# Performance work log

Measured on AMD Instinct MI355X. Metric: run time of the kernel, lower is better.

The kernel has to match this reference:

```python
import jax, jax.numpy as jnp
import numpy as np

B, H, W, C_IN, C_QK = 8, 64, 64, 256, 32


def setup_inputs() -> dict:
    key = jax.random.key(0)
    ks = jax.random.split(key, 5)
    x = jax.random.normal(ks[0], (B, H, W, C_IN), dtype=jnp.float32)
    Wq = jax.random.normal(ks[1], (C_IN, C_QK), dtype=jnp.float32) * 0.05
    bq = jnp.zeros((C_QK,), dtype=jnp.float32)
    Wk = jax.random.normal(ks[2], (C_IN, C_QK), dtype=jnp.float32) * 0.05
    bk = jnp.zeros((C_QK,), dtype=jnp.float32)
    Wv = jax.random.normal(ks[3], (C_IN, C_IN), dtype=jnp.float32) * 0.05
    bv = jnp.zeros((C_IN,), dtype=jnp.float32)
    gamma = jax.random.normal(ks[4], (1,), dtype=jnp.float32)
    return {"x": x, "Wq": Wq, "bq": bq, "Wk": Wk, "bk": bk, "Wv": Wv, "bv": bv, "gamma": gamma}


def reference(x, Wq, bq, Wk, bk, Wv, bv, gamma):
    b, h, w, c_in = x.shape
    n = h * w
    xt = x.reshape(b, n, c_in)                      # tokens: (B, N, C_in)
    # 1x1 convs == per-token channel matmuls
    q = xt @ Wq + bq                                # (B, N, Cqk)
    k = xt @ Wk + bk                                # (B, N, Cqk)
    v = xt @ Wv + bv                                # (B, N, C_in)
    energy = jnp.einsum('bnc,bmc->bnm', q, k)       # (B, N, N)
    attn = jax.nn.softmax(energy, axis=-1)
    # original: out = (V^T @ A^T)^T == A @ V
    out = jnp.einsum('bnm,bmc->bnc', attn, v)       # (B, N, C_in)
    out = out.reshape(b, h, w, c_in)
    out = gamma * out + x                           # residual with learned scale
    return jnp.mean(out, axis=-1)                   # channel-mean pool -> (B, H, W)
```

## Files before the change

### kernel.cpp

```cpp
#include <hip/hip_runtime.h>
#include <hip/hip_bf16.h>


typedef _Float16 half8  __attribute__((ext_vector_type(8)));
typedef _Float16 half4v __attribute__((ext_vector_type(4)));
typedef float    f32x4  __attribute__((ext_vector_type(4)));

#define LOG2E 1.4426950408889634f

#if __has_builtin(__builtin_amdgcn_exp2f)
#define EXP2(x) __builtin_amdgcn_exp2f(x)
#else
#define EXP2(x) exp2f(x)
#endif

__global__ __launch_bounds__(256) void prep_kernel(
    const float* __restrict__ Wq, const float* __restrict__ Wk,
    const float* __restrict__ Wv, const float* __restrict__ bv,
    _Float16* __restrict__ Wfr, float* __restrict__ wvbar, float* __restrict__ bvbar)
{
  int bid = blockIdx.x, tid = threadIdx.x;
  if (bid < 64) {
    int col = bid, c = tid;
    float v = (col < 32) ? Wq[c * 32 + col] : Wk[c * 32 + (col - 32)];
    int ch = c >> 5, quad = (c >> 3) & 3, j = c & 7;
    Wfr[(size_t)((ch * 4 + quad) * 64 + col) * 8 + j] = (_Float16)v;
  } else if (bid < 128) {
    int row = (bid - 64) * 4 + (tid >> 6);
    int lane = tid & 63;
    const float* p = Wv + (size_t)row * 256 + lane * 4;
    float s = p[0] + p[1] + p[2] + p[3];
    #pragma unroll
    for (int off = 32; off >= 1; off >>= 1) s += __shfl_xor(s, off);
    if (lane == 0) wvbar[row] = s * (1.0f / 256.0f);
  } else {
    if (tid < 64) {
      const float* p = bv + tid * 4;
      float s = p[0] + p[1] + p[2] + p[3];
      #pragma unroll
      for (int off = 32; off >= 1; off >>= 1) s += __shfl_xor(s, off);
      if (tid == 0) bvbar[0] = s * (1.0f / 256.0f);
    }
  }
}

__global__ __launch_bounds__(256) void proj_kernel(
    const float* __restrict__ x, const _Float16* __restrict__ Wfr,
    const float* __restrict__ bq, const float* __restrict__ bk,
    const float* __restrict__ wvbar, const float* __restrict__ bvbar,
    _Float16* __restrict__ Qh, _Float16* __restrict__ Kh,
    float* __restrict__ vbarO, float* __restrict__ xbarO)
{
  __shared__ _Float16 XT[64 * 264];
  int tid = threadIdx.x, blk = blockIdx.x;
  size_t tok0 = (size_t)blk * 64;

  const float4* xg4 = (const float4*)x;
  #pragma unroll
  for (int i = 0; i < 16; ++i) {
    int f = i * 256 + tid;
    int tok = f >> 6, c4 = f & 63;
    float4 v = xg4[(size_t)blk * 4096 + f];
    half4v h;
    h.x = (_Float16)v.x; h.y = (_Float16)v.y; h.z = (_Float16)v.z; h.w = (_Float16)v.w;
    *(half4v*)&XT[tok * 264 + c4 * 4] = h;
  }
  __syncthreads();

  if (tid < 64) {
    float vs = 0.f, xs = 0.f;
    #pragma unroll 4
    for (int g = 0; g < 32; ++g) {
      half8 h = *(const half8*)&XT[tid * 264 + g * 8];
      #pragma unroll
      for (int j = 0; j < 8; ++j) {
        float xv = (float)h[j];
        vs += xv * wvbar[g * 8 + j];
        xs += xv;
      }
    }
    vbarO[tok0 + tid] = vs + bvbar[0];
    xbarO[tok0 + tid] = xs * (1.0f / 256.0f);
  }

  int lane = tid & 63, w = tid >> 6;
  int l15 = lane & 15, quad = lane >> 4;
  f32x4 acc[4] = {(f32x4){0,0,0,0},(f32x4){0,0,0,0},(f32x4){0,0,0,0},(f32x4){0,0,0,0}};
  #pragma unroll
  for (int ch = 0; ch < 8; ++ch) {
    half8 a = *(const half8*)&XT[(w * 16 + l15) * 264 + ch * 32 + quad * 8];
    #pragma unroll
    for (int ct = 0; ct < 4; ++ct) {
      half8 bf = *(const half8*)(Wfr + (size_t)((ch * 4 + quad) * 64 + ct * 16 + l15) * 8);
      acc[ct] = __builtin_amdgcn_mfma_f32_16x16x32_f16(a, bf, acc[ct], 0, 0, 0);
    }
  }
  #pragma unroll
  for (int ct = 0; ct < 4; ++ct) {
    int col = ct * 16 + l15;
    #pragma unroll
    for (int r = 0; r < 4; ++r) {
      int token = w * 16 + quad * 4 + r;
      if (ct < 2) {
        float val = (acc[ct][r] + bq[col]) * LOG2E;
        Qh[(tok0 + token) * 32 + col] = (_Float16)val;
      } else {
        float val = acc[ct][r] + bk[col - 32];
        Kh[(tok0 + token) * 32 + (col - 32)] = (_Float16)val;
      }
    }
  }
}

__global__ __launch_bounds__(256) void flash_kernel(
    const _Float16* __restrict__ Qh, const _Float16* __restrict__ Kh,
    const float* __restrict__ vbar, const float* __restrict__ xbar,
    const float* __restrict__ gamma, float* __restrict__ out)
{
  int tid = threadIdx.x, blk = blockIdx.x;
  int b = blk >> 6, qt = blk & 63;
  int lane = tid & 63, w = tid >> 6;
  int l15 = lane & 15, quad = lane >> 4;

  const _Float16* Qb = Qh + (size_t)b * 4096 * 32;
  const _Float16* Kb = Kh + (size_t)b * 4096 * 32;
  const float* vb = vbar + (size_t)b * 4096;

  int qrow = qt * 64 + w * 16 + l15;
  half8 aq = *(const half8*)(Qb + (size_t)qrow * 32 + quad * 8);

  float lacc[4] = {0, 0, 0, 0}, oacc[4] = {0, 0, 0, 0};
  const f32x4 cinit = {-88.f, -88.f, -88.f, -88.f};

  const _Float16* kfrag = Kb + (size_t)l15 * 32 + quad * 8;
  const float* vfrag = vb + l15;

  #pragma unroll 2
  for (int kt = 0; kt < 64; ++kt) {
    half8 bk8[4];
    float vbl[4];
    #pragma unroll
    for (int ct = 0; ct < 4; ++ct) {
      bk8[ct] = *(const half8*)(kfrag + (size_t)(kt * 64 + ct * 16) * 32);
      vbl[ct] = vfrag[kt * 64 + ct * 16];
    }
    f32x4 sc[4];
    #pragma unroll
    for (int ct = 0; ct < 4; ++ct)
      sc[ct] = __builtin_amdgcn_mfma_f32_16x16x32_f16(aq, bk8[ct], cinit, 0, 0, 0);
    #pragma unroll
    for (int r = 0; r < 4; ++r) {
      float p0 = EXP2(sc[0][r]), p1 = EXP2(sc[1][r]);
      float p2 = EXP2(sc[2][r]), p3 = EXP2(sc[3][r]);
      lacc[r] += (p0 + p1) + (p2 + p3);
      oacc[r] += ((p0 * vbl[0] + p1 * vbl[1]) + (p2 * vbl[2] + p3 * vbl[3]));
    }
  }

  #pragma unroll
  for (int r = 0; r < 4; ++r) {
    #pragma unroll
    for (int off = 1; off < 16; off <<= 1) {
      lacc[r] += __shfl_xor(lacc[r], off);
      oacc[r] += __shfl_xor(oacc[r], off);
    }
  }
  if (l15 == 0) {
    float g = gamma[0];
    #pragma unroll
    for (int r = 0; r < 4; ++r) {
      int row = qt * 64 + w * 16 + quad * 4 + r;
      out[(size_t)b * 4096 + row] = g * (oacc[r] / lacc[r]) + xbar[(size_t)b * 4096 + row];
    }
  }
}

extern "C" void kernel_launch(void* const* d_in, const int* in_sizes, int n_in,
                              void* d_out, int out_size, void* d_ws, size_t ws_size,
                              hipStream_t stream)
{
  const float* x     = (const float*)d_in[0];
  const float* Wq    = (const float*)d_in[1];
  const float* bq    = (const float*)d_in[2];
  const float* Wk    = (const float*)d_in[3];
  const float* bk    = (const float*)d_in[4];
  const float* Wv    = (const float*)d_in[5];
  const float* bv    = (const float*)d_in[6];
  const float* gamma = (const float*)d_in[7];
  float* out = (float*)d_out;

  char* ws = (char*)d_ws;
  _Float16* Wfr  = (_Float16*)(ws);
  float* wvbar   = (float*)(ws + 32768);
  float* bvbar   = (float*)(ws + 33792);
  _Float16* Qh   = (_Float16*)(ws + 65536);
  _Float16* Kh   = (_Float16*)(ws + 65536 + 2097152);
  float* vbarA   = (float*)(ws + 65536 + 4194304);
  float* xbarA   = (float*)(ws + 65536 + 4194304 + 131072);

  prep_kernel<<<129, 256, 0, stream>>>(Wq, Wk, Wv, bv, Wfr, wvbar, bvbar);
  proj_kernel<<<512, 256, 0, stream>>>(x, Wfr, bq, bk, wvbar, bvbar, Qh, Kh, vbarA, xbarA);
  flash_kernel<<<512, 256, 0, stream>>>(Qh, Kh, vbarA, xbarA, gamma, out);
}
```

Measured before the change: 125.8 us.

## Split flash attention over two key halves and combine partials in a new kernel

Measured after the change: 129.0 us. +2.5%, slower.

```diff
diff --git a/kernel.cpp b/kernel.cpp
--- a/kernel.cpp
+++ b/kernel.cpp
@@ -5,6 +5,7 @@
 typedef _Float16 half8  __attribute__((ext_vector_type(8)));
 typedef _Float16 half4v __attribute__((ext_vector_type(4)));
 typedef float    f32x4  __attribute__((ext_vector_type(4)));
+typedef float    f32x2  __attribute__((ext_vector_type(2)));
 
 #define LOG2E 1.4426950408889634f
 
@@ -112,13 +113,15 @@
   }
 }
 
-__global__ __launch_bounds__(256) void flash_kernel(
+__global__ __launch_bounds__(256, 4) void flash_kernel(
     const _Float16* __restrict__ Qh, const _Float16* __restrict__ Kh,
-    const float* __restrict__ vbar, const float* __restrict__ xbar,
-    const float* __restrict__ gamma, float* __restrict__ out)
+    const float* __restrict__ vbar,
+    float* __restrict__ lpart, float* __restrict__ opart)
 {
   int tid = threadIdx.x, blk = blockIdx.x;
-  int b = blk >> 6, qt = blk & 63;
+  int b = blk >> 7;
+  int qt = (blk >> 1) & 63;
+  int ks = blk & 1;
   int lane = tid & 63, w = tid >> 6;
   int l15 = lane & 15, quad = lane >> 4;
 
@@ -129,14 +132,16 @@
   int qrow = qt * 64 + w * 16 + l15;
   half8 aq = *(const half8*)(Qb + (size_t)qrow * 32 + quad * 8);
 
-  float lacc[4] = {0, 0, 0, 0}, oacc[4] = {0, 0, 0, 0};
+  f32x2 l2[4], o2[4];
+  #pragma unroll
+  for (int r = 0; r < 4; ++r) { l2[r] = (f32x2){0, 0}; o2[r] = (f32x2){0, 0}; }
   const f32x4 cinit = {-88.f, -88.f, -88.f, -88.f};
 
-  const _Float16* kfrag = Kb + (size_t)l15 * 32 + quad * 8;
-  const float* vfrag = vb + l15;
+  const _Float16* kfrag = Kb + ((size_t)ks * 2048 + l15) * 32 + quad * 8;
+  const float* vfrag = vb + ks * 2048 + l15;
 
   #pragma unroll 2
-  for (int kt = 0; kt < 64; ++kt) {
+  for (int kt = 0; kt < 32; ++kt) {
     half8 bk8[4];
     float vbl[4];
     #pragma unroll
@@ -148,14 +153,21 @@
     #pragma unroll
     for (int ct = 0; ct < 4; ++ct)
       sc[ct] = __builtin_amdgcn_mfma_f32_16x16x32_f16(aq, bk8[ct], cinit, 0, 0, 0);
+    f32x2 vA = {vbl[0], vbl[1]}, vB = {vbl[2], vbl[3]};
     #pragma unroll
     for (int r = 0; r < 4; ++r) {
       float p0 = EXP2(sc[0][r]), p1 = EXP2(sc[1][r]);
       float p2 = EXP2(sc[2][r]), p3 = EXP2(sc[3][r]);
-      lacc[r] += (p0 + p1) + (p2 + p3);
-      oacc[r] += ((p0 * vbl[0] + p1 * vbl[1]) + (p2 * vbl[2] + p3 * vbl[3]));
-    }
-  }
+      f32x2 pA = {p0, p1}, pB = {p2, p3};
+      l2[r] += pA + pB;
+      o2[r] += pA * vA;
+      o2[r] += pB * vB;
+    }
+  }
+
+  float lacc[4], oacc[4];
+  #pragma unroll
+  for (int r = 0; r < 4; ++r) { lacc[r] = l2[r].x + l2[r].y; oacc[r] = o2[r].x + o2[r].y; }
 
   #pragma unroll
   for (int r = 0; r < 4; ++r) {
@@ -166,13 +178,25 @@
     }
   }
   if (l15 == 0) {
-    float g = gamma[0];
     #pragma unroll
     for (int r = 0; r < 4; ++r) {
       int row = qt * 64 + w * 16 + quad * 4 + r;
-      out[(size_t)b * 4096 + row] = g * (oacc[r] / lacc[r]) + xbar[(size_t)b * 4096 + row];
-    }
-  }
+      size_t g = (size_t)b * 4096 + row;
+      lpart[(size_t)ks * 32768 + g] = lacc[r];
+      opart[(size_t)ks * 32768 + g] = oacc[r];
+    }
+  }
+}
+
+__global__ __launch_bounds__(256) void combine_kernel(
+    const float* __restrict__ lpart, const float* __restrict__ opart,
+    const float* __restrict__ xbar, const float* __restrict__ gamma,
+    float* __restrict__ out)
+{
+  int i = blockIdx.x * 256 + threadIdx.x;
+  float l = lpart[i] + lpart[32768 + i];
+  float o = opart[i] + opart[32768 + i];
+  out[i] = gamma[0] * (o / l) + xbar[i];
 }
 
 extern "C" void kernel_launch(void* const* d_in, const int* in_sizes, int n_in,
@@ -197,8 +221,11 @@
   _Float16* Kh   = (_Float16*)(ws + 65536 + 2097152);
   float* vbarA   = (float*)(ws + 65536 + 4194304);
   float* xbarA   = (float*)(ws + 65536 + 4194304 + 131072);
+  float* lpart   = (float*)(ws + 65536 + 4194304 + 262144);
+  float* opart   = (float*)(ws + 65536 + 4194304 + 524288);
 
   prep_kernel<<<129, 256, 0, stream>>>(Wq, Wk, Wv, bv, Wfr, wvbar, bvbar);
   proj_kernel<<<512, 256, 0, stream>>>(x, Wfr, bq, bk, wvbar, bvbar, Qh, Kh, vbarA, xbarA);
-  flash_kernel<<<512, 256, 0, stream>>>(Qh, Kh, vbarA, xbarA, gamma, out);
-}
+  flash_kernel<<<1024, 256, 0, stream>>>(Qh, Kh, vbarA, lpart, opart);
+  combine_kernel<<<128, 256, 0, stream>>>(lpart, opart, xbarA, gamma, out);
+}
```

## Fuse prep, projection and attention kernels into one persistent kernel with grid barriers

Applied to the files above, without the earlier changes.

Result: slower. 229.0 us (+82.0%).

```diff
diff --git a/kernel.cpp b/kernel.cpp
--- a/kernel.cpp
+++ b/kernel.cpp
@@ -1,5 +1,4 @@
 #include <hip/hip_runtime.h>
-#include <hip/hip_bf16.h>
 
 
 typedef _Float16 half8  __attribute__((ext_vector_type(8)));
@@ -14,26 +13,53 @@
 #define EXP2(x) exp2f(x)
 #endif
 
-__global__ __launch_bounds__(256) void prep_kernel(
-    const float* __restrict__ Wq, const float* __restrict__ Wk,
+#define NBLOCKS 512
+
+__device__ __forceinline__ void grid_barrier(int* cnt) {
+  __syncthreads();
+  if (threadIdx.x == 0) {
+    __threadfence();
+    __hip_atomic_fetch_add(cnt, 1, __ATOMIC_ACQ_REL, __HIP_MEMORY_SCOPE_AGENT);
+    long t = 0;
+    while (__hip_atomic_load(cnt, __ATOMIC_ACQUIRE, __HIP_MEMORY_SCOPE_AGENT) < NBLOCKS) {
+      if (++t > (1L << 26)) break;
+      __builtin_amdgcn_s_sleep(1);
+    }
+    __threadfence();
+  }
+  __syncthreads();
+}
+
+__global__ __launch_bounds__(256, 2) void fused_kernel(
+    const float* __restrict__ x,
+    const float* __restrict__ Wq, const float* __restrict__ bq,
+    const float* __restrict__ Wk, const float* __restrict__ bk,
     const float* __restrict__ Wv, const float* __restrict__ bv,
-    _Float16* __restrict__ Wfr, float* __restrict__ wvbar, float* __restrict__ bvbar)
+    const float* __restrict__ gamma,
+    _Float16* __restrict__ Wfr, float* __restrict__ wvbar, float* __restrict__ bvbar,
+    _Float16* __restrict__ Qh, _Float16* __restrict__ Kh,
+    float* __restrict__ vbarA, float* __restrict__ xbarA,
+    int* __restrict__ gbar,
+    float* __restrict__ out)
 {
-  int bid = blockIdx.x, tid = threadIdx.x;
-  if (bid < 64) {
-    int col = bid, c = tid;
+  __shared__ _Float16 XT[64 * 264];
+  int tid = threadIdx.x, blk = blockIdx.x;
+  int lane = tid & 63, w = tid >> 6;
+  int l15 = lane & 15, quad = lane >> 4;
+
+  if (blk < 64) {
+    int col = blk, c = tid;
     float v = (col < 32) ? Wq[c * 32 + col] : Wk[c * 32 + (col - 32)];
-    int ch = c >> 5, quad = (c >> 3) & 3, j = c & 7;
-    Wfr[(size_t)((ch * 4 + quad) * 64 + col) * 8 + j] = (_Float16)v;
-  } else if (bid < 128) {
-    int row = (bid - 64) * 4 + (tid >> 6);
-    int lane = tid & 63;
+    int ch = c >> 5, qd = (c >> 3) & 3, j = c & 7;
+    Wfr[(size_t)((ch * 4 + qd) * 64 + col) * 8 + j] = (_Float16)v;
+  } else if (blk < 128) {
+    int row = (blk - 64) * 4 + w;
     const float* p = Wv + (size_t)row * 256 + lane * 4;
     float s = p[0] + p[1] + p[2] + p[3];
     #pragma unroll
     for (int off = 32; off >= 1; off >>= 1) s += __shfl_xor(s, off);
     if (lane == 0) wvbar[row] = s * (1.0f / 256.0f);
-  } else {
+  } else if (blk == 128) {
     if (tid < 64) {
       const float* p = bv + tid * 4;
       float s = p[0] + p[1] + p[2] + p[3];
@@ -42,135 +68,122 @@
       if (tid == 0) bvbar[0] = s * (1.0f / 256.0f);
     }
   }
-}
-
-__global__ __launch_bounds__(256) void proj_kernel(
-    const float* __restrict__ x, const _Float16* __restrict__ Wfr,
-    const float* __restrict__ bq, const float* __restrict__ bk,
-    const float* __restrict__ wvbar, const float* __restrict__ bvbar,
-    _Float16* __restrict__ Qh, _Float16* __restrict__ Kh,
-    float* __restrict__ vbarO, float* __restrict__ xbarO)
-{
-  __shared__ _Float16 XT[64 * 264];
-  int tid = threadIdx.x, blk = blockIdx.x;
-  size_t tok0 = (size_t)blk * 64;
-
-  const float4* xg4 = (const float4*)x;
-  #pragma unroll
-  for (int i = 0; i < 16; ++i) {
-    int f = i * 256 + tid;
-    int tok = f >> 6, c4 = f & 63;
-    float4 v = xg4[(size_t)blk * 4096 + f];
-    half4v h;
-    h.x = (_Float16)v.x; h.y = (_Float16)v.y; h.z = (_Float16)v.z; h.w = (_Float16)v.w;
-    *(half4v*)&XT[tok * 264 + c4 * 4] = h;
-  }
-  __syncthreads();
-
-  if (tid < 64) {
-    float vs = 0.f, xs = 0.f;
-    #pragma unroll 4
-    for (int g = 0; g < 32; ++g) {
-      half8 h = *(const half8*)&XT[tid * 264 + g * 8];
-      #pragma unroll
-      for (int j = 0; j < 8; ++j) {
-        float xv = (float)h[j];
-        vs += xv * wvbar[g * 8 + j];
-        xs += xv;
-      }
-    }
-    vbarO[tok0 + tid] = vs + bvbar[0];
-    xbarO[tok0 + tid] = xs * (1.0f / 256.0f);
-  }
-
-  int lane = tid & 63, w = tid >> 6;
-  int l15 = lane & 15, quad = lane >> 4;
-  f32x4 acc[4] = {(f32x4){0,0,0,0},(f32x4){0,0,0,0},(f32x4){0,0,0,0},(f32x4){0,0,0,0}};
-  #pragma unroll
-  for (int ch = 0; ch < 8; ++ch) {
-    half8 a = *(const half8*)&XT[(w * 16 + l15) * 264 + ch * 32 + quad * 8];
+
+  grid_barrier(gbar + 0);
+
+  {
+    size_t tok0 = (size_t)blk * 64;
+
+    const float4* xg4 = (const float4*)x;
+    #pragma unroll
+    for (int i = 0; i < 16; ++i) {
+      int f = i * 256 + tid;
+      int tok = f >> 6, c4 = f & 63;
+      float4 v = xg4[(size_t)blk * 4096 + f];
+      half4v h;
+      h.x = (_Float16)v.x; h.y = (_Float16)v.y; h.z = (_Float16)v.z; h.w = (_Float16)v.w;
+      *(half4v*)&XT[tok * 264 + c4 * 4] = h;
+    }
+    __syncthreads();
+
+    if (tid < 64) {
+      float vs = 0.f, xs = 0.f;
+      #pragma unroll 4
+      for (int g = 0; g < 32; ++g) {
+        half8 h = *(const half8*)&XT[tid * 264 + g * 8];
+        #pragma unroll
+        for (int j = 0; j < 8; ++j) {
+          float xv = (float)h[j];
+          vs += xv * wvbar[g * 8 + j];
+          xs += xv;
+        }
+      }
+      vbarA[tok0 + tid] = vs + bvbar[0];
+      xbarA[tok0 + tid] = xs * (1.0f / 256.0f);
+    }
+
+    f32x4 acc[4] = {(f32x4){0,0,0,0},(f32x4){0,0,0,0},(f32x4){0,0,0,0},(f32x4){0,0,0,0}};
+    #pragma unroll
+    for (int ch = 0; ch < 8; ++ch) {
+      half8 a = *(const half8*)&XT[(w * 16 + l15) * 264 + ch * 32 + quad * 8];
+      #pragma unroll
+      for (int ct = 0; ct < 4; ++ct) {
+        half8 bf = *(const half8*)(Wfr + (size_t)((ch * 4 + quad) * 64 + ct * 16 + l15) * 8);
+        acc[ct] = __builtin_amdgcn_mfma_f32_16x16x32_f16(a, bf, acc[ct], 0, 0, 0);
+      }
+    }
     #pragma unroll
     for (int ct = 0; ct < 4; ++ct) {
-      half8 bf = *(const half8*)(Wfr + (size_t)((ch * 4 + quad) * 64 + ct * 16 + l15) * 8);
-      acc[ct] = __builtin_amdgcn_mfma_f32_16x16x32_f16(a, bf, acc[ct], 0, 0, 0);
-    }
-  }
-  #pragma unroll
-  for (int ct = 0; ct < 4; ++ct) {
-    int col = ct * 16 + l15;
+      int col = ct * 16 + l15;
+      #pragma unroll
+      for (int r = 0; r < 4; ++r) {
+        int token = w * 16 + quad * 4 + r;
+        if (ct < 2) {
+          float val = (acc[ct][r] + bq[col]) * LOG2E;
+          Qh[(tok0 + token) * 32 + col] = (_Float16)val;
+        } else {
+          float val = acc[ct][r] + bk[col - 32];
+          Kh[(tok0 + token) * 32 + (col - 32)] = (_Float16)val;
+        }
+      }
+    }
+  }
+
+  grid_barrier(gbar + 1);
+
+  {
+    int b = blk >> 6, qt = blk & 63;
+
+    const _Float16* Qb = Qh + (size_t)b * 4096 * 32;
+    const _Float16* Kb = Kh + (size_t)b * 4096 * 32;
+    const float* vb = vbarA + (size_t)b * 4096;
+
+    int qrow = qt * 64 + w * 16 + l15;
+    half8 aq = *(const half8*)(Qb + (size_t)qrow * 32 + quad * 8);
+
+    float lacc[4] = {0, 0, 0, 0}, oacc[4] = {0, 0, 0, 0};
+    const f32x4 cinit = {-88.f, -88.f, -88.f, -88.f};
+
+    const _Float16* kfrag = Kb + (size_t)l15 * 32 + quad * 8;
+    const float* vfrag = vb + l15;
+
+    #pragma unroll 2
+    for (int kt = 0; kt < 64; ++kt) {
+      half8 bk8[4];
+      float vbl[4];
+      #pragma unroll
+      for (int ct = 0; ct < 4; ++ct) {
+        bk8[ct] = *(const half8*)(kfrag + (size_t)(kt * 64 + ct * 16) * 32);
+        vbl[ct] = vfrag[kt * 64 + ct * 16];
+      }
+      f32x4 sc[4];
+      #pragma unroll
+      for (int ct = 0; ct < 4; ++ct)
+        sc[ct] = __builtin_amdgcn_mfma_f32_16x16x32_f16(aq, bk8[ct], cinit, 0, 0, 0);
+      #pragma unroll
+      for (int r = 0; r < 4; ++r) {
+        float p0 = EXP2(sc[0][r]), p1 = EXP2(sc[1][r]);
+        float p2 = EXP2(sc[2][r]), p3 = EXP2(sc[3][r]);
+        lacc[r] += (p0 + p1) + (p2 + p3);
+        oacc[r] += ((p0 * vbl[0] + p1 * vbl[1]) + (p2 * vbl[2] + p3 * vbl[3]));
+      }
+    }
+
     #pragma unroll
     for (int r = 0; r < 4; ++r) {
-      int token = w * 16 + quad * 4 + r;
-      if (ct < 2) {
-        float val = (acc[ct][r] + bq[col]) * LOG2E;
-        Qh[(tok0 + token) * 32 + col] = (_Float16)val;
-      } else {
-        float val = acc[ct][r] + bk[col - 32];
-        Kh[(tok0 + token) * 32 + (col - 32)] = (_Float16)val;
-      }
-    }
-  }
-}
-
-__global__ __launch_bounds__(256) void flash_kernel(
-    const _Float16* __restrict__ Qh, const _Float16* __restrict__ Kh,
-    const float* __restrict__ vbar, const float* __restrict__ xbar,
-    const float* __restrict__ gamma, float* __restrict__ out)
-{
-  int tid = threadIdx.x, blk = blockIdx.x;
-  int b = blk >> 6, qt = blk & 63;
-  int lane = tid & 63, w = tid >> 6;
-  int l15 = lane & 15, quad = lane >> 4;
-
-  const _Float16* Qb = Qh + (size_t)b * 4096 * 32;
-  const _Float16* Kb = Kh + (size_t)b * 4096 * 32;
-  const float* vb = vbar + (size_t)b * 4096;
-
-  int qrow = qt * 64 + w * 16 + l15;
-  half8 aq = *(const half8*)(Qb + (size_t)qrow * 32 + quad * 8);
-
-  float lacc[4] = {0, 0, 0, 0}, oacc[4] = {0, 0, 0, 0};
-  const f32x4 cinit = {-88.f, -88.f, -88.f, -88.f};
-
-  const _Float16* kfrag = Kb + (size_t)l15 * 32 + quad * 8;
-  const float* vfrag = vb + l15;
-
-  #pragma unroll 2
-  for (int kt = 0; kt < 64; ++kt) {
-    half8 bk8[4];
-    float vbl[4];
-    #pragma unroll
-    for (int ct = 0; ct < 4; ++ct) {
-      bk8[ct] = *(const half8*)(kfrag + (size_t)(kt * 64 + ct * 16) * 32);
-      vbl[ct] = vfrag[kt * 64 + ct * 16];
-    }
-    f32x4 sc[4];
-    #pragma unroll
-    for (int ct = 0; ct < 4; ++ct)
-      sc[ct] = __builtin_amdgcn_mfma_f32_16x16x32_f16(aq, bk8[ct], cinit, 0, 0, 0);
-    #pragma unroll
-    for (int r = 0; r < 4; ++r) {
-      float p0 = EXP2(sc[0][r]), p1 = EXP2(sc[1][r]);
-      float p2 = EXP2(sc[2][r]), p3 = EXP2(sc[3][r]);
-      lacc[r] += (p0 + p1) + (p2 + p3);
-      oacc[r] += ((p0 * vbl[0] + p1 * vbl[1]) + (p2 * vbl[2] + p3 * vbl[3]));
-    }
-  }
-
-  #pragma unroll
-  for (int r = 0; r < 4; ++r) {
-    #pragma unroll
-    for (int off = 1; off < 16; off <<= 1) {
-      lacc[r] += __shfl_xor(lacc[r], off);
-      oacc[r] += __shfl_xor(oacc[r], off);
-    }
-  }
-  if (l15 == 0) {
-    float g = gamma[0];
-    #pragma unroll
-    for (int r = 0; r < 4; ++r) {
-      int row = qt * 64 + w * 16 + quad * 4 + r;
-      out[(size_t)b * 4096 + row] = g * (oacc[r] / lacc[r]) + xbar[(size_t)b * 4096 + row];
+      #pragma unroll
+      for (int off = 1; off < 16; off <<= 1) {
+        lacc[r] += __shfl_xor(lacc[r], off);
+        oacc[r] += __shfl_xor(oacc[r], off);
+      }
+    }
+    if (l15 == 0) {
+      float g = gamma[0];
+      #pragma unroll
+      for (int r = 0; r < 4; ++r) {
+        int row = qt * 64 + w * 16 + quad * 4 + r;
+        out[(size_t)b * 4096 + row] = g * (oacc[r] / lacc[r]) + xbarA[(size_t)b * 4096 + row];
+      }
     }
   }
 }
@@ -197,8 +210,10 @@
   _Float16* Kh   = (_Float16*)(ws + 65536 + 2097152);
   float* vbarA   = (float*)(ws + 65536 + 4194304);
   float* xbarA   = (float*)(ws + 65536 + 4194304 + 131072);
-
-  prep_kernel<<<129, 256, 0, stream>>>(Wq, Wk, Wv, bv, Wfr, wvbar, bvbar);
-  proj_kernel<<<512, 256, 0, stream>>>(x, Wfr, bq, bk, wvbar, bvbar, Qh, Kh, vbarA, xbarA);
-  flash_kernel<<<512, 256, 0, stream>>>(Qh, Kh, vbarA, xbarA, gamma, out);
+  int*   gbar    = (int*)(ws + 8388608);
+
+  hipMemsetAsync(gbar, 0, 2 * sizeof(int), stream);
+  fused_kernel<<<NBLOCKS, 256, 0, stream>>>(
+      x, Wq, bq, Wk, bk, Wv, bv, gamma,
+      Wfr, wvbar, bvbar, Qh, Kh, vbarA, xbarA, gbar, out);
 }
```

## Split key range across warps with all query rows per warp and LDS reduce

Applied to the files above, without the earlier changes.

New measurement: 118.0 us. -6.2%, faster.

```diff
diff --git a/kernel.cpp b/kernel.cpp
--- a/kernel.cpp
+++ b/kernel.cpp
@@ -117,6 +117,8 @@
     const float* __restrict__ vbar, const float* __restrict__ xbar,
     const float* __restrict__ gamma, float* __restrict__ out)
 {
+  __shared__ float Lp[4][64];
+  __shared__ float Op[4][64];
   int tid = threadIdx.x, blk = blockIdx.x;
   int b = blk >> 6, qt = blk & 63;
   int lane = tid & 63, w = tid >> 6;
@@ -126,17 +128,23 @@
   const _Float16* Kb = Kh + (size_t)b * 4096 * 32;
   const float* vb = vbar + (size_t)b * 4096;
 
-  int qrow = qt * 64 + w * 16 + l15;
-  half8 aq = *(const half8*)(Qb + (size_t)qrow * 32 + quad * 8);
-
-  float lacc[4] = {0, 0, 0, 0}, oacc[4] = {0, 0, 0, 0};
+  half8 aq[4];
+  #pragma unroll
+  for (int af = 0; af < 4; ++af)
+    aq[af] = *(const half8*)(Qb + (size_t)(qt * 64 + af * 16 + l15) * 32 + quad * 8);
+
+  float lacc[4][4], oacc[4][4];
+  #pragma unroll
+  for (int af = 0; af < 4; ++af)
+    #pragma unroll
+    for (int r = 0; r < 4; ++r) { lacc[af][r] = 0.f; oacc[af][r] = 0.f; }
   const f32x4 cinit = {-88.f, -88.f, -88.f, -88.f};
 
-  const _Float16* kfrag = Kb + (size_t)l15 * 32 + quad * 8;
-  const float* vfrag = vb + l15;
+  const _Float16* kfrag = Kb + ((size_t)w * 1024 + l15) * 32 + quad * 8;
+  const float* vfrag = vb + w * 1024 + l15;
 
   #pragma unroll 2
-  for (int kt = 0; kt < 64; ++kt) {
+  for (int kt = 0; kt < 16; ++kt) {
     half8 bk8[4];
     float vbl[4];
     #pragma unroll
@@ -144,34 +152,48 @@
       bk8[ct] = *(const half8*)(kfrag + (size_t)(kt * 64 + ct * 16) * 32);
       vbl[ct] = vfrag[kt * 64 + ct * 16];
     }
-    f32x4 sc[4];
-    #pragma unroll
-    for (int ct = 0; ct < 4; ++ct)
-      sc[ct] = __builtin_amdgcn_mfma_f32_16x16x32_f16(aq, bk8[ct], cinit, 0, 0, 0);
+    #pragma unroll
+    for (int af = 0; af < 4; ++af) {
+      f32x4 sc[4];
+      #pragma unroll
+      for (int ct = 0; ct < 4; ++ct)
+        sc[ct] = __builtin_amdgcn_mfma_f32_16x16x32_f16(aq[af], bk8[ct], cinit, 0, 0, 0);
+      #pragma unroll
+      for (int r = 0; r < 4; ++r) {
+        float p0 = EXP2(sc[0][r]), p1 = EXP2(sc[1][r]);
+        float p2 = EXP2(sc[2][r]), p3 = EXP2(sc[3][r]);
+        lacc[af][r] += (p0 + p1) + (p2 + p3);
+        oacc[af][r] += ((p0 * vbl[0] + p1 * vbl[1]) + (p2 * vbl[2] + p3 * vbl[3]));
+      }
+    }
+  }
+
+  #pragma unroll
+  for (int af = 0; af < 4; ++af)
     #pragma unroll
     for (int r = 0; r < 4; ++r) {
-      float p0 = EXP2(sc[0][r]), p1 = EXP2(sc[1][r]);
-      float p2 = EXP2(sc[2][r]), p3 = EXP2(sc[3][r]);
-      lacc[r] += (p0 + p1) + (p2 + p3);
-      oacc[r] += ((p0 * vbl[0] + p1 * vbl[1]) + (p2 * vbl[2] + p3 * vbl[3]));
-    }
-  }
-
-  #pragma unroll
-  for (int r = 0; r < 4; ++r) {
-    #pragma unroll
-    for (int off = 1; off < 16; off <<= 1) {
-      lacc[r] += __shfl_xor(lacc[r], off);
-      oacc[r] += __shfl_xor(oacc[r], off);
-    }
-  }
+      #pragma unroll
+      for (int off = 1; off < 16; off <<= 1) {
+        lacc[af][r] += __shfl_xor(lacc[af][r], off);
+        oacc[af][r] += __shfl_xor(oacc[af][r], off);
+      }
+    }
+
   if (l15 == 0) {
-    float g = gamma[0];
-    #pragma unroll
-    for (int r = 0; r < 4; ++r) {
-      int row = qt * 64 + w * 16 + quad * 4 + r;
-      out[(size_t)b * 4096 + row] = g * (oacc[r] / lacc[r]) + xbar[(size_t)b * 4096 + row];
-    }
+    #pragma unroll
+    for (int af = 0; af < 4; ++af)
+      #pragma unroll
+      for (int r = 0; r < 4; ++r) {
+        Lp[w][af * 16 + quad * 4 + r] = lacc[af][r];
+        Op[w][af * 16 + quad * 4 + r] = oacc[af][r];
+      }
+  }
+  __syncthreads();
+  if (tid < 64) {
+    float l = (Lp[0][tid] + Lp[1][tid]) + (Lp[2][tid] + Lp[3][tid]);
+    float o = (Op[0][tid] + Op[1][tid]) + (Op[2][tid] + Op[3][tid]);
+    size_t g = (size_t)b * 4096 + qt * 64 + tid;
+    out[g] = gamma[0] * (o / l) + xbar[g];
   }
 }
 
```
